# Kernel tuning notes

Measured on AMD Instinct MI355X. Metric: run time of the kernel, lower is better.

Reference implementation:

```python
import jax, jax.numpy as jnp
import numpy as np

NEG_INF = -9.0e15  # matches torch's -9000000000000000.0 mask value
ALPHA = 0.2        # leaky_relu negative slope
F_OUT = 128


def setup_inputs() -> dict:
    key = jax.random.key(0)
    k1, k2, k3, k4 = jax.random.split(key, 4)
    B, N, F_IN = 4, 4096, 128
    x = jax.random.normal(k1, (B, N, F_IN), dtype=jnp.float32)
    adj = jax.random.randint(k2, (B, N, N), 0, 2, dtype=jnp.int32)
    # xavier-uniform-like init for params
    lim_W = float(np.sqrt(6.0 / (F_IN + F_OUT)))
    W = jax.random.uniform(k3, (F_IN, F_OUT), jnp.float32, -lim_W, lim_W)
    lim_a = float(np.sqrt(6.0 / (2 * F_OUT + 1)))
    a = jax.random.uniform(k4, (2 * F_OUT, 1), jnp.float32, -lim_a, lim_a)
    return {"x": x, "adj": adj, "W": W, "a": a}


def reference(x, adj, W, a):
    # x: [B, N, Fin], adj: [B, N, N], W: [Fin, Fout], a: [2*Fout, 1]
    Wh = jnp.matmul(x, W)                       # [B, N, Fout]
    Wh1 = jnp.matmul(Wh, a[:F_OUT, :])          # [B, N, 1]
    Wh2 = jnp.matmul(Wh, a[F_OUT:, :])          # [B, N, 1]
    # NOTE: faithful to the source: e = Wh1 + Wh2 is [B, N, 1] (no transpose)
    e = jax.nn.leaky_relu(Wh1 + Wh2, negative_slope=ALPHA)
    # broadcast e across last dim of adj, mask, row-softmax over axis 2
    scores = jnp.where(adj > 0, e, jnp.float32(NEG_INF))  # [B, N, N]
    attention = jax.nn.softmax(scores, axis=2)
    # dropout with p=0.0 / eval mode -> identity
    h_prime = jnp.matmul(attention, Wh)         # [B, N, Fout]
    return h_prime
```

## Files before the change

kernel.cpp:

```cpp
#include <hip/hip_runtime.h>
#include <hip/hip_bf16.h>

typedef unsigned short u16;
typedef unsigned int u32;
typedef short bf16x8 __attribute__((ext_vector_type(8)));
typedef float f32x4 __attribute__((ext_vector_type(4)));

__device__ inline float bf2f(u16 u) { return __uint_as_float(((u32)u) << 16); }
__device__ inline u16 f2bf(float f) {
    u32 x = __float_as_uint(f);
    return (u16)((x + 0x7FFFu + ((x >> 16) & 1u)) >> 16);
}

__global__ __launch_bounds__(256) void k_gemm1(const float* __restrict__ x,
                                               const float* __restrict__ W,
                                               u16* __restrict__ Wht,
                                               float* __restrict__ S) {
    __shared__ __align__(16) u16 Wt[128][136];
    const int t = threadIdx.x;
    {
        int k = t >> 1;
        int f0 = (t & 1) * 64;
        const float4* wp = reinterpret_cast<const float4*>(W + k * 128 + f0);
#pragma unroll
        for (int q = 0; q < 16; ++q) {
            float4 v = wp[q];
            int f = f0 + q * 4;
            Wt[f + 0][k] = f2bf(v.x);
            Wt[f + 1][k] = f2bf(v.y);
            Wt[f + 2][k] = f2bf(v.z);
            Wt[f + 3][k] = f2bf(v.w);
        }
    }
    __syncthreads();

    const int w = t >> 6, l = t & 63;
    const int lr = l & 15, lg = l >> 4;
    const int fh = (w & 1) * 64;
    const int jh = (w >> 1) * 64;
    const int j0 = blockIdx.x * 128;

    f32x4 acc[4][4];
#pragma unroll
    for (int m = 0; m < 4; ++m)
#pragma unroll
        for (int n = 0; n < 4; ++n) acc[m][n] = (f32x4){0.f, 0.f, 0.f, 0.f};

#pragma unroll
    for (int ks = 0; ks < 4; ++ks) {
        bf16x8 a[4], bb[4];
#pragma unroll
        for (int m = 0; m < 4; ++m)
            a[m] = *reinterpret_cast<const bf16x8*>(&Wt[fh + m * 16 + lr][ks * 32 + lg * 8]);
#pragma unroll
        for (int n = 0; n < 4; ++n) {
            int j = j0 + jh + n * 16 + lr;
            const float* xp = x + (size_t)j * 128 + ks * 32 + lg * 8;
            float4 v0 = *reinterpret_cast<const float4*>(xp);
            float4 v1 = *reinterpret_cast<const float4*>(xp + 4);
            bf16x8 bv;
            bv[0] = (short)f2bf(v0.x); bv[1] = (short)f2bf(v0.y);
            bv[2] = (short)f2bf(v0.z); bv[3] = (short)f2bf(v0.w);
            bv[4] = (short)f2bf(v1.x); bv[5] = (short)f2bf(v1.y);
            bv[6] = (short)f2bf(v1.z); bv[7] = (short)f2bf(v1.w);
            bb[n] = bv;
        }
#pragma unroll
        for (int m = 0; m < 4; ++m)
#pragma unroll
            for (int n = 0; n < 4; ++n)
                acc[m][n] = __builtin_amdgcn_mfma_f32_16x16x32_bf16(a[m], bb[n], acc[m][n], 0, 0, 0);
    }

    const int bb_ = blockIdx.x >> 5;
    const int jj = (blockIdx.x & 31) * 128;
    u16* base = Wht + ((size_t)bb_ << 19);
    float* Sb = S + bb_ * 128;
#pragma unroll
    for (int m = 0; m < 4; ++m) {
        int f = fh + m * 16 + lg * 4;
#pragma unroll
        for (int n = 0; n < 4; ++n) {
            int j = jj + jh + n * 16 + lr;
#pragma unroll
            for (int r = 0; r < 4; ++r)
                base[(size_t)(f + r) * 4096 + j] = f2bf(acc[m][n][r]);
        }
#pragma unroll
        for (int r = 0; r < 4; ++r) {
            float sj = 0.f;
#pragma unroll
            for (int n = 0; n < 4; ++n) sj += acc[m][n][r];
            sj += __shfl_xor(sj, 1);
            sj += __shfl_xor(sj, 2);
            sj += __shfl_xor(sj, 4);
            sj += __shfl_xor(sj, 8);
            if (lr == 0) atomicAdd(&Sb[f + r], sj);
        }
    }
}

__global__ __launch_bounds__(256) void k_gemm2(const int* __restrict__ adj,
                                               const u16* __restrict__ Wht,
                                               const float* __restrict__ S,
                                               float* __restrict__ out) {
    __shared__ __align__(16) u16 As[2][32][72];
    __shared__ __align__(16) u16 Bs[2][128][72];
    __shared__ int cnt_lds[32];
    __shared__ float inv_lds[32];

    const int t = threadIdx.x;
    const int raw = blockIdx.x;
    const int swz = (raw & 7) * 64 + (raw >> 3);
    const int b = swz >> 7;
    const int i0 = (swz & 127) * 32;
    const int* adjb = adj + ((size_t)b << 24) + (size_t)i0 * 4096;
    const u16* whb = Wht + ((size_t)b << 19);

    const int ai = t >> 3;
    const int ak = (t & 7) * 8;
    const int bf = t >> 1;
    const int bk = (t & 1) * 32;

    int4 av[2];
    uint4 bv[4];
    int cnt = 0;

    auto issue = [&](int k0) {
        const int4* ap = reinterpret_cast<const int4*>(adjb + (size_t)ai * 4096 + k0 + ak);
        av[0] = ap[0]; av[1] = ap[1];
        const uint4* bp = reinterpret_cast<const uint4*>(whb + (size_t)bf * 4096 + k0 + bk);
        bv[0] = bp[0]; bv[1] = bp[1]; bv[2] = bp[2]; bv[3] = bp[3];
    };
    auto convert_write = [&](int buf) {
        u32 u[4];
#pragma unroll
        for (int q = 0; q < 2; ++q) {
            int4 v = av[q];
            cnt += (v.x > 0) + (v.y > 0) + (v.z > 0) + (v.w > 0);
            u[q * 2 + 0] = ((v.x > 0) ? 0x3F80u : 0u) | (((v.y > 0) ? 0x3F80u : 0u) << 16);
            u[q * 2 + 1] = ((v.z > 0) ? 0x3F80u : 0u) | (((v.w > 0) ? 0x3F80u : 0u) << 16);
        }
        *reinterpret_cast<uint4*>(&As[buf][ai][ak]) = make_uint4(u[0], u[1], u[2], u[3]);
        uint4* bw = reinterpret_cast<uint4*>(&Bs[buf][bf][bk]);
        bw[0] = bv[0]; bw[1] = bv[1]; bw[2] = bv[2]; bw[3] = bv[3];
    };

    const int w = t >> 6, l = t & 63;
    const int lr = l & 15, lg = l >> 4;
    const int ir = w & 1;
    const int fr0 = (w >> 1) * 4;

    f32x4 acc[4];
#pragma unroll
    for (int n = 0; n < 4; ++n) acc[n] = (f32x4){0.f, 0.f, 0.f, 0.f};

    issue(0);
    convert_write(0);
    __syncthreads();

    for (int kt = 0; kt < 64; ++kt) {
        const int cur = kt & 1;
        const bool pre = (kt + 1 < 64);
        if (pre) issue((kt + 1) * 64);

#pragma unroll
        for (int ks = 0; ks < 2; ++ks) {
            bf16x8 a = *reinterpret_cast<const bf16x8*>(&As[cur][ir * 16 + lr][ks * 32 + lg * 8]);
#pragma unroll
            for (int n = 0; n < 4; ++n) {
                bf16x8 bbv = *reinterpret_cast<const bf16x8*>(&Bs[cur][(fr0 + n) * 16 + lr][ks * 32 + lg * 8]);
                acc[n] = __builtin_amdgcn_mfma_f32_16x16x32_bf16(a, bbv, acc[n], 0, 0, 0);
            }
        }

        if (pre) convert_write(cur ^ 1);
        __syncthreads();
    }

    int c = cnt + __shfl_xor(cnt, 1);
    c += __shfl_xor(c, 2);
    c += __shfl_xor(c, 4);
    if ((t & 7) == 0) cnt_lds[ai] = c;
    __syncthreads();
    if (t < 32) {
        int cc = cnt_lds[t];
        inv_lds[t] = (cc > 0) ? (1.0f / (float)cc) : 0.0f;
    }
    __syncthreads();

    float* ob = out + (((size_t)b * 4096) + i0) * 128;
#pragma unroll
    for (int n = 0; n < 4; ++n) {
        int f = (fr0 + n) * 16 + lr;
        float sv = S[b * 128 + f] * (1.0f / 4096.0f);
#pragma unroll
        for (int r = 0; r < 4; ++r) {
            int il = ir * 16 + lg * 4 + r;
            int cc = cnt_lds[il];
            float v = (cc > 0) ? acc[n][r] * inv_lds[il] : sv;
            ob[(size_t)il * 128 + f] = v;
        }
    }
}

extern "C" void kernel_launch(void* const* d_in, const int* in_sizes, int n_in,
                              void* d_out, int out_size, void* d_ws, size_t ws_size,
                              hipStream_t stream) {
    const float* x = (const float*)d_in[0];
    const int* adj = (const int*)d_in[1];
    const float* W = (const float*)d_in[2];
    float* out = (float*)d_out;

    u16* Wht = (u16*)d_ws;
    float* S = (float*)((char*)d_ws + (size_t)4 * 128 * 4096 * 2);

    hipMemsetAsync(S, 0, 512 * sizeof(float), stream);
    k_gemm1<<<128, 256, 0, stream>>>(x, W, Wht, S);
    k_gemm2<<<512, 256, 0, stream>>>(adj, Wht, S, out);
}
```

Before: 478.0 us.

## Split K across blocks, enlarge row tile, load Wh directly to registers

The aggregation kernel now processes 64 rows per block with a two-way split of the reduction dimension. Partial sums and per-row neighbour counts go to workspace, and a new finalize kernel combines them. The Wh operand is read straight from global memory into registers instead of being staged through LDS, which cuts LDS traffic and doubles MFMA reuse of each B fragment. In exchange it adds a partial-sum buffer write and read, atomics for counts, and an extra kernel launch.

```diff
diff --git a/kernel.cpp b/kernel.cpp
--- a/kernel.cpp
+++ b/kernel.cpp
@@ -102,106 +102,127 @@
 
 __global__ __launch_bounds__(256) void k_gemm2(const int* __restrict__ adj,
                                                const u16* __restrict__ Wht,
-                                               const float* __restrict__ S,
-                                               float* __restrict__ out) {
-    __shared__ __align__(16) u16 As[2][32][72];
-    __shared__ __align__(16) u16 Bs[2][128][72];
-    __shared__ int cnt_lds[32];
-    __shared__ float inv_lds[32];
+                                               float* __restrict__ part,
+                                               int* __restrict__ cnt) {
+    __shared__ __align__(16) u16 As[2][64][72];
 
     const int t = threadIdx.x;
     const int raw = blockIdx.x;
     const int swz = (raw & 7) * 64 + (raw >> 3);
-    const int b = swz >> 7;
-    const int i0 = (swz & 127) * 32;
-    const int* adjb = adj + ((size_t)b << 24) + (size_t)i0 * 4096;
-    const u16* whb = Wht + ((size_t)b << 19);
-
-    const int ai = t >> 3;
-    const int ak = (t & 7) * 8;
-    const int bf = t >> 1;
-    const int bk = (t & 1) * 32;
-
-    int4 av[2];
-    uint4 bv[4];
-    int cnt = 0;
-
-    auto issue = [&](int k0) {
-        const int4* ap = reinterpret_cast<const int4*>(adjb + (size_t)ai * 4096 + k0 + ak);
-        av[0] = ap[0]; av[1] = ap[1];
-        const uint4* bp = reinterpret_cast<const uint4*>(whb + (size_t)bf * 4096 + k0 + bk);
-        bv[0] = bp[0]; bv[1] = bp[1]; bv[2] = bp[2]; bv[3] = bp[3];
+    const int b   = swz >> 7;
+    const int ksp = (swz >> 6) & 1;
+    const int i0  = (swz & 63) * 64;
+    const int koff = ksp * 2048;
+
+    const int* adjb = adj + ((size_t)b << 24) + (size_t)i0 * 4096 + koff;
+    const u16* whb  = Wht + ((size_t)b << 19) + koff;
+
+    const int ai = t >> 2;
+    const int aq = t & 3;
+    const int* aptr = adjb + (size_t)ai * 4096 + aq * 16;
+
+    int4 av[4];
+    int cntv = 0;
+
+    auto issueA = [&](int kt) {
+        const int4* p = reinterpret_cast<const int4*>(aptr + kt * 64);
+        av[0] = p[0]; av[1] = p[1]; av[2] = p[2]; av[3] = p[3];
     };
-    auto convert_write = [&](int buf) {
-        u32 u[4];
-#pragma unroll
-        for (int q = 0; q < 2; ++q) {
+    auto convertA = [&](int buf) {
+        u32 u[8];
+#pragma unroll
+        for (int q = 0; q < 4; ++q) {
             int4 v = av[q];
-            cnt += (v.x > 0) + (v.y > 0) + (v.z > 0) + (v.w > 0);
+            cntv += (v.x > 0) + (v.y > 0) + (v.z > 0) + (v.w > 0);
             u[q * 2 + 0] = ((v.x > 0) ? 0x3F80u : 0u) | (((v.y > 0) ? 0x3F80u : 0u) << 16);
             u[q * 2 + 1] = ((v.z > 0) ? 0x3F80u : 0u) | (((v.w > 0) ? 0x3F80u : 0u) << 16);
         }
-        *reinterpret_cast<uint4*>(&As[buf][ai][ak]) = make_uint4(u[0], u[1], u[2], u[3]);
-        uint4* bw = reinterpret_cast<uint4*>(&Bs[buf][bf][bk]);
-        bw[0] = bv[0]; bw[1] = bv[1]; bw[2] = bv[2]; bw[3] = bv[3];
+        *reinterpret_cast<uint4*>(&As[buf][ai][aq * 16]) = make_uint4(u[0], u[1], u[2], u[3]);
+        *reinterpret_cast<uint4*>(&As[buf][ai][aq * 16 + 8]) = make_uint4(u[4], u[5], u[6], u[7]);
     };
 
     const int w = t >> 6, l = t & 63;
     const int lr = l & 15, lg = l >> 4;
-    const int ir = w & 1;
+    const int ir0 = (w & 1) * 2;
     const int fr0 = (w >> 1) * 4;
 
-    f32x4 acc[4];
-#pragma unroll
-    for (int n = 0; n < 4; ++n) acc[n] = (f32x4){0.f, 0.f, 0.f, 0.f};
-
-    issue(0);
-    convert_write(0);
+    const u16* bptr0 = whb + (size_t)((fr0 + 0) * 16 + lr) * 4096 + lg * 8;
+    const u16* bptr1 = whb + (size_t)((fr0 + 1) * 16 + lr) * 4096 + lg * 8;
+    const u16* bptr2 = whb + (size_t)((fr0 + 2) * 16 + lr) * 4096 + lg * 8;
+    const u16* bptr3 = whb + (size_t)((fr0 + 3) * 16 + lr) * 4096 + lg * 8;
+
+    f32x4 acc[2][4];
+#pragma unroll
+    for (int m = 0; m < 2; ++m)
+#pragma unroll
+        for (int n = 0; n < 4; ++n) acc[m][n] = (f32x4){0.f, 0.f, 0.f, 0.f};
+
+    issueA(0);
+    convertA(0);
     __syncthreads();
 
-    for (int kt = 0; kt < 64; ++kt) {
+    for (int kt = 0; kt < 32; ++kt) {
         const int cur = kt & 1;
-        const bool pre = (kt + 1 < 64);
-        if (pre) issue((kt + 1) * 64);
+        bf16x8 bb0[4], bb1[4];
+        bb0[0] = *reinterpret_cast<const bf16x8*>(bptr0 + kt * 64);
+        bb0[1] = *reinterpret_cast<const bf16x8*>(bptr1 + kt * 64);
+        bb0[2] = *reinterpret_cast<const bf16x8*>(bptr2 + kt * 64);
+        bb0[3] = *reinterpret_cast<const bf16x8*>(bptr3 + kt * 64);
+        bb1[0] = *reinterpret_cast<const bf16x8*>(bptr0 + kt * 64 + 32);
+        bb1[1] = *reinterpret_cast<const bf16x8*>(bptr1 + kt * 64 + 32);
+        bb1[2] = *reinterpret_cast<const bf16x8*>(bptr2 + kt * 64 + 32);
+        bb1[3] = *reinterpret_cast<const bf16x8*>(bptr3 + kt * 64 + 32);
+        if (kt + 1 < 32) issueA(kt + 1);
 
 #pragma unroll
         for (int ks = 0; ks < 2; ++ks) {
-            bf16x8 a = *reinterpret_cast<const bf16x8*>(&As[cur][ir * 16 + lr][ks * 32 + lg * 8]);
+            bf16x8 a0 = *reinterpret_cast<const bf16x8*>(&As[cur][(ir0 + 0) * 16 + lr][ks * 32 + lg * 8]);
+            bf16x8 a1 = *reinterpret_cast<const bf16x8*>(&As[cur][(ir0 + 1) * 16 + lr][ks * 32 + lg * 8]);
 #pragma unroll
             for (int n = 0; n < 4; ++n) {
-                bf16x8 bbv = *reinterpret_cast<const bf16x8*>(&Bs[cur][(fr0 + n) * 16 + lr][ks * 32 + lg * 8]);
-                acc[n] = __builtin_amdgcn_mfma_f32_16x16x32_bf16(a, bbv, acc[n], 0, 0, 0);
+                bf16x8 bv = ks ? bb1[n] : bb0[n];
+                acc[0][n] = __builtin_amdgcn_mfma_f32_16x16x32_bf16(a0, bv, acc[0][n], 0, 0, 0);
+                acc[1][n] = __builtin_amdgcn_mfma_f32_16x16x32_bf16(a1, bv, acc[1][n], 0, 0, 0);
             }
         }
 
-        if (pre) convert_write(cur ^ 1);
+        if (kt + 1 < 32) convertA(cur ^ 1);
         __syncthreads();
     }
 
-    int c = cnt + __shfl_xor(cnt, 1);
+    int c = cntv + __shfl_xor(cntv, 1);
     c += __shfl_xor(c, 2);
-    c += __shfl_xor(c, 4);
-    if ((t & 7) == 0) cnt_lds[ai] = c;
-    __syncthreads();
-    if (t < 32) {
-        int cc = cnt_lds[t];
-        inv_lds[t] = (cc > 0) ? (1.0f / (float)cc) : 0.0f;
-    }
-    __syncthreads();
-
-    float* ob = out + (((size_t)b * 4096) + i0) * 128;
-#pragma unroll
-    for (int n = 0; n < 4; ++n) {
-        int f = (fr0 + n) * 16 + lr;
-        float sv = S[b * 128 + f] * (1.0f / 4096.0f);
-#pragma unroll
-        for (int r = 0; r < 4; ++r) {
-            int il = ir * 16 + lg * 4 + r;
-            int cc = cnt_lds[il];
-            float v = (cc > 0) ? acc[n][r] * inv_lds[il] : sv;
-            ob[(size_t)il * 128 + f] = v;
-        }
-    }
+    if ((t & 3) == 0) atomicAdd(&cnt[b * 4096 + i0 + ai], c);
+
+    float* pb = part + ((size_t)ksp << 21) + ((size_t)b * 4096 + i0) * 128;
+#pragma unroll
+    for (int m = 0; m < 2; ++m) {
+#pragma unroll
+        for (int n = 0; n < 4; ++n) {
+            int f = (fr0 + n) * 16 + lr;
+#pragma unroll
+            for (int r = 0; r < 4; ++r) {
+                int il = (ir0 + m) * 16 + lg * 4 + r;
+                pb[(size_t)il * 128 + f] = acc[m][n][r];
+            }
+        }
+    }
+}
+
+__global__ __launch_bounds__(256) void k_fin(const float* __restrict__ part,
+                                             const int* __restrict__ cnt,
+                                             const float* __restrict__ S,
+                                             float* __restrict__ out) {
+    int e = blockIdx.x * 256 + threadIdx.x;
+    int f = e & 127;
+    int row = e >> 7;
+    int b = row >> 12;
+    int c = cnt[row];
+    float p = part[e] + part[e + (1 << 21)];
+    float v;
+    if (c > 0) v = p / (float)c;
+    else       v = S[b * 128 + f] * (1.0f / 4096.0f);
+    out[e] = v;
 }
 
 extern "C" void kernel_launch(void* const* d_in, const int* in_sizes, int n_in,
@@ -212,10 +233,14 @@
     const float* W = (const float*)d_in[2];
     float* out = (float*)d_out;
 
-    u16* Wht = (u16*)d_ws;
-    float* S = (float*)((char*)d_ws + (size_t)4 * 128 * 4096 * 2);
-
-    hipMemsetAsync(S, 0, 512 * sizeof(float), stream);
+    char* wsb = (char*)d_ws;
+    float* S    = (float*)(wsb);
+    int*   cnt  = (int*)(wsb + 4096);
+    float* part = (float*)(wsb + (1u << 20));
+    u16*   Wht  = (u16*)(wsb + (1u << 25));
+
+    hipMemsetAsync(wsb, 0, 4096 + 65536, stream);
     k_gemm1<<<128, 256, 0, stream>>>(x, W, Wht, S);
-    k_gemm2<<<512, 256, 0, stream>>>(adj, Wht, S, out);
-}
+    k_gemm2<<<512, 256, 0, stream>>>(adj, Wht, part, cnt);
+    k_fin<<<8192, 256, 0, stream>>>(part, cnt, S, out);
+}
```

New measurement: 413.5 us. 1.16x faster.
